# Kernel optimization log

Hardware: AMD Instinct MI355X
Metric: run time of the kernel (lower is better)

The kernel has to match this reference:

```python
import jax, jax.numpy as jnp
import numpy as np

B, CIN, COUT, H, W = 4, 256, 256, 64, 64
KH, KW = 3, 3
STRIDE, PAD = 1, 1
K = KH * KW


def setup_inputs() -> dict:
    key = jax.random.key(0)
    k1, k2, k3 = jax.random.split(key, 3)
    x = jax.random.normal(k1, (B, CIN, H, W), dtype=jnp.float32)
    # small offset weights -> offsets of O(1) pixel, realistic near init
    offset_w = jax.random.normal(k2, (2 * K, CIN, KH, KW), dtype=jnp.float32) * 0.01
    offset_b = jnp.zeros((2 * K,), dtype=jnp.float32)
    dcn_w = jax.random.normal(k3, (COUT, CIN, KH, KW), dtype=jnp.float32) * (1.0 / np.sqrt(CIN * K))
    dcn_b = jnp.zeros((COUT,), dtype=jnp.float32)
    return {"x": x, "offset_w": offset_w, "offset_b": offset_b, "dcn_w": dcn_w, "dcn_b": dcn_b}


def _conv2d(x, w, b):
    y = jax.lax.conv_general_dilated(
        x, w, window_strides=(STRIDE, STRIDE),
        padding=((PAD, PAD), (PAD, PAD)),
        dimension_numbers=("NCHW", "OIHW", "NCHW"))
    return y + b[None, :, None, None]


def _bilinear_gather(x, py, px):
    """x: [B,C,H,W]; py,px: [B,K,Ho,Wo] float sample coords.
    Zero padding outside image (torchvision deform_conv2d semantics).
    Returns [B,C,K,Ho,Wo]."""
    Bb, C, Hin, Win = x.shape
    y0 = jnp.floor(py); x0 = jnp.floor(px)
    wy1 = py - y0; wx1 = px - x0
    y0i = y0.astype(jnp.int32); x0i = x0.astype(jnp.int32)
    x_flat = x.reshape(Bb, C, Hin * Win)

    def corner(yi, xi, wgt):
        valid = (yi >= 0) & (yi < Hin) & (xi >= 0) & (xi < Win)
        yc = jnp.clip(yi, 0, Hin - 1)
        xc = jnp.clip(xi, 0, Win - 1)
        idx = (yc * Win + xc).reshape(Bb, -1)  # [B, K*Ho*Wo]
        vals = jax.vmap(lambda xf, ix: jnp.take(xf, ix, axis=1))(x_flat, idx)
        vals = vals.reshape(Bb, C, *yi.shape[1:])  # [B,C,K,Ho,Wo]
        w_eff = jnp.where(valid, wgt, 0.0)[:, None]  # [B,1,K,Ho,Wo]
        return vals * w_eff

    out = corner(y0i, x0i, (1.0 - wy1) * (1.0 - wx1))
    out = out + corner(y0i, x0i + 1, (1.0 - wy1) * wx1)
    out = out + corner(y0i + 1, x0i, wy1 * (1.0 - wx1))
    out = out + corner(y0i + 1, x0i + 1, wy1 * wx1)
    return out


def _deformable_block(x, offset_w, offset_b, dcn_w, dcn_b):
    offset = _conv2d(x, offset_w, offset_b)  # [B, 2K, Ho, Wo]
    Bb, _, Ho, Wo = offset.shape
    off = offset.reshape(Bb, K, 2, Ho, Wo)
    dy, dx = off[:, :, 0], off[:, :, 1]  # torchvision: (y, x) interleaved per tap

    ky = jnp.repeat(jnp.arange(KH), KW).astype(jnp.float32)  # [K]
    kx = jnp.tile(jnp.arange(KW), KH).astype(jnp.float32)    # [K]
    base_y = (jnp.arange(Ho, dtype=jnp.float32) * STRIDE - PAD)[None, :, None] + ky[:, None, None]  # [K,Ho,1]
    base_x = (jnp.arange(Wo, dtype=jnp.float32) * STRIDE - PAD)[None, None, :] + kx[:, None, None]  # [K,1,Wo]
    py = base_y[None] + dy  # [B,K,Ho,Wo]
    px = base_x[None] + dx

    patches = _bilinear_gather(x, py, px)  # [B,C,K,Ho,Wo]
    wk = dcn_w.reshape(COUT, CIN, K)
    out = jnp.einsum("bckhw,ock->bohw", patches, wk)
    return out + dcn_b[None, :, None, None]


def reference(x, offset_w, offset_b, dcn_w, dcn_b):
    return _deformable_block(x, offset_w, offset_b, dcn_w, dcn_b)
```

## Files before the change

kernel.cpp:

```cpp
#include <hip/hip_runtime.h>

#define BB 4
#define CIN 256
#define COUT 256
#define HH 64
#define WW 64
#define KK 9
#define OC2 18
#define KTOT (CIN * KK)

typedef __attribute__((ext_vector_type(8))) _Float16 h8;
typedef __attribute__((ext_vector_type(4))) float f32x4;

static __device__ __forceinline__ h8 splat_pk(unsigned pk) {
    union { unsigned u[4]; h8 h; } s;
    s.u[0] = pk; s.u[1] = pk; s.u[2] = pk; s.u[3] = pk;
    return s.h;
}

__global__ __launch_bounds__(256) void prework_kernel(
    const float* __restrict__ x, const float* __restrict__ ow,
    const float* __restrict__ dw,
    _Float16* __restrict__ xT, _Float16* __restrict__ bp,
    _Float16* __restrict__ bow)
{
    const int bid = blockIdx.x;
    const int t = threadIdx.x;
    if (bid < 1024) {
        const int b = bid >> 8, y = (bid >> 2) & 63, c0 = (bid & 3) * 64;
        __shared__ float tile[64][65];
#pragma unroll
        for (int r = 0; r < 16; ++r) {
            int idx = r * 256 + t;
            int c = idx >> 6, w = idx & 63;
            tile[c][w] = x[(((size_t)(b * CIN + c0 + c)) << 12) + (y << 6) + w];
        }
        __syncthreads();
        const int px = t >> 2;
#pragma unroll
        for (int half = 0; half < 2; ++half) {
            int cc = (t & 3) + half * 4;
            union { _Float16 h[8]; uint4 q; } u;
#pragma unroll
            for (int j = 0; j < 8; ++j) u.h[j] = (_Float16)tile[cc * 8 + j][px];
            size_t el = (((size_t)(b << 12)) + (y << 6) + px) * 256 + c0 + cc * 8;
            *(uint4*)&xT[el] = u.q;
        }
    } else if (bid < 1312) {
        int wid = (bid - 1024) * 256 + t;
        int T = wid >> 10;
        int r = wid & 1023;
        int cotile = r >> 6, lane = r & 63;
        int co = cotile * 16 + (lane & 15);
        int kbase = T * 32 + ((lane >> 4) & 3) * 8;
        union { _Float16 h[8]; uint4 q; } u;
#pragma unroll
        for (int j = 0; j < 8; ++j) {
            int k = kbase + j;
            int c = k & 255, kk = k >> 8;
            u.h[j] = (_Float16)dw[co * KTOT + c * KK + kk];
        }
        *(uint4*)&bp[(size_t)wid * 8] = u.q;
    } else {
        int wid = (bid - 1312) * 256 + t;
        int T = wid >> 7;
        int r = wid & 127;
        int lane = r & 63;
        int oc = ((r >> 6) << 4) + (lane & 15);
        int kbase = T * 32 + ((lane >> 4) & 3) * 8;
        union { _Float16 h[8]; uint4 q; } u;
#pragma unroll
        for (int j = 0; j < 8; ++j) {
            int k = kbase + j;
            int c = k & 255, kk = k >> 8;
            u.h[j] = (oc < OC2) ? (_Float16)ow[oc * KTOT + c * KK + kk] : (_Float16)0.f;
        }
        *(uint4*)&bow[(size_t)wid * 8] = u.q;
    }
}

__global__ __launch_bounds__(512) void offset_mfma_kernel(
    const _Float16* __restrict__ xT, const _Float16* __restrict__ bow,
    float* __restrict__ opart)
{
    const int bid = blockIdx.x;
    const int m_blk = bid >> 1, kh = bid & 1;
    const int b = m_blk >> 5;
    const int pxbase = (m_blk & 31) * 128;
    const int tid = threadIdx.x;
    const int lane = tid & 63, wv = tid >> 6;
    const int colg = lane & 15, kg = lane >> 4;

    const int pxl = pxbase + (wv << 4) + colg;
    const int py = pxl >> 6, pxx = pxl & 63;

    const _Float16* xb = xT + ((size_t)b << 20);

    auto GLOAD = [&](int T, h8& R) {
        int kk = T >> 3;
        int ky = kk / 3, kx = kk - 3 * (kk / 3);
        int yy = py + ky - 1, xx = pxx + kx - 1;
        h8 v = {0, 0, 0, 0, 0, 0, 0, 0};
        if ((unsigned)yy < HH && (unsigned)xx < WW)
            v = *(const h8*)(xb + ((((yy << 6) + xx) << 8) + ((T & 7) << 5) + (kg << 3)));
        R = v;
    };
    auto BLOAD = [&](int T, uint4* br) {
#pragma unroll
        for (int nj = 0; nj < 2; ++nj)
            br[nj] = *(const uint4*)&bow[(size_t)(((T << 1) + nj) * 64 + lane) * 8];
    };

    f32x4 acc[2];
    { f32x4 z = {0.f, 0.f, 0.f, 0.f}; acc[0] = z; acc[1] = z; }

    const int Tb = kh * 36;
    h8 E, F;
    uint4 bA[2], bB[2];

    GLOAD(Tb, E);
    BLOAD(Tb, bA);
    for (int r = 0; r < 36; r += 2) {
        GLOAD(Tb + r + 1, F);
        BLOAD(Tb + r + 1, bB);
        {
            union { uint4 q; h8 h; } u0, u1;
            u0.q = bA[0]; u1.q = bA[1];
            acc[0] = __builtin_amdgcn_mfma_f32_16x16x32_f16(E, u0.h, acc[0], 0, 0, 0);
            acc[1] = __builtin_amdgcn_mfma_f32_16x16x32_f16(E, u1.h, acc[1], 0, 0, 0);
        }
        if (r + 2 < 36) { GLOAD(Tb + r + 2, E); BLOAD(Tb + r + 2, bA); }
        {
            union { uint4 q; h8 h; } u0, u1;
            u0.q = bB[0]; u1.q = bB[1];
            acc[0] = __builtin_amdgcn_mfma_f32_16x16x32_f16(F, u0.h, acc[0], 0, 0, 0);
            acc[1] = __builtin_amdgcn_mfma_f32_16x16x32_f16(F, u1.h, acc[1], 0, 0, 0);
        }
    }

    const int pxb = pxbase + (wv << 4) + kg * 4;
#pragma unroll
    for (int nj = 0; nj < 2; ++nj) {
        int oc = nj * 16 + colg;
        if (oc < OC2) {
            float4 o;
            o.x = acc[nj][0]; o.y = acc[nj][1];
            o.z = acc[nj][2]; o.w = acc[nj][3];
            *(float4*)&opart[(((size_t)((kh * BB + b) * OC2 + oc)) << 12) + pxb] = o;
        }
    }
}

__global__ __launch_bounds__(512, 2) void dcn_mfma_kernel(
    const _Float16* __restrict__ xT, const float* __restrict__ opart,
    const float* __restrict__ ob, const _Float16* __restrict__ bp,
    const float* __restrict__ db, float* __restrict__ out)
{
    __shared__ __align__(16) _Float16 Asl[2][1088 * 8];
    __shared__ __align__(8) uint2 twp[576];
    __shared__ __align__(8) uint2 tih[576];

    int P = blockIdx.x;
    int L = (P & 7) * 64 + (P >> 3);
    const int m_blk = L >> 1, n0 = L & 1;
    const int b = m_blk >> 6;
    const int rowbase = (m_blk & 63) * 64;

    const int tid = threadIdx.x;
    const int lane = tid & 63;
    const int wn = tid >> 6;
    const int colg = lane & 15, kg = lane >> 4;

    const int g_px = tid >> 3;
    const int g_cgp = tid & 7;
    const int g_ebase = g_px * 9;
    const int g_w0 = g_px * 17 + g_cgp;

    const float* op0 = opart + (((size_t)(b * OC2)) << 12);
    const float* op1 = opart + (((size_t)((BB + b) * OC2)) << 12);
    for (int e = tid; e < 576; e += 512) {
        int p = e / 9, kk = e - (e / 9) * 9;
        int pxl = rowbase + p;
        int y = pxl >> 6, xx = pxl & 63;
        float dy = op0[((size_t)(2 * kk) << 12) + pxl]
                 + op1[((size_t)(2 * kk) << 12) + pxl] + ob[2 * kk];
        float dx = op0[((size_t)(2 * kk + 1) << 12) + pxl]
                 + op1[((size_t)(2 * kk + 1) << 12) + pxl] + ob[2 * kk + 1];
        int ky = kk / 3, kx = kk - 3 * (kk / 3);
        float sy = (float)(y - 1 + ky) + dy;
        float sx = (float)(xx - 1 + kx) + dx;
        float fy = floorf(sy), fx = floorf(sx);
        int y0 = (int)fy, x0 = (int)fx;
        float wy1 = sy - fy, wx1 = sx - fx;
        float wy0 = 1.f - wy1, wx0 = 1.f - wx1;
        bool vy0 = (unsigned)y0 < HH, vy1 = (unsigned)(y0 + 1) < HH;
        bool vx0 = (unsigned)x0 < WW, vx1 = (unsigned)(x0 + 1) < WW;
        _Float16 w00 = (_Float16)((vy0 && vx0) ? wy0 * wx0 : 0.f);
        _Float16 w01 = (_Float16)((vy0 && vx1) ? wy0 * wx1 : 0.f);
        _Float16 w10 = (_Float16)((vy1 && vx0) ? wy1 * wx0 : 0.f);
        _Float16 w11 = (_Float16)((vy1 && vx1) ? wy1 * wx1 : 0.f);
        union { _Float16 h[2]; unsigned u; } pk2;
        uint2 W;
        pk2.h[0] = w00; pk2.h[1] = w01; W.x = pk2.u;
        pk2.h[0] = w10; pk2.h[1] = w11; W.y = pk2.u;
        twp[e] = W;
        int y0c = min(max(y0, 0), HH - 1), y1c = min(max(y0 + 1, 0), HH - 1);
        int x0c = min(max(x0, 0), WW - 1), x1c = min(max(x0 + 1, 0), WW - 1);
        unsigned i00 = (unsigned)((y0c << 6) + x0c);
        unsigned i01 = (unsigned)((y0c << 6) + x1c);
        unsigned i10 = (unsigned)((y1c << 6) + x0c);
        unsigned i11 = (unsigned)((y1c << 6) + x1c);
        tih[e] = make_uint2(i00 | (i01 << 16), i10 | (i11 << 16));
    }
    __syncthreads();

    const char* xbyte = (const char*)(xT + ((size_t)b << 20));

    auto AGLOAD = [&](int st, h8* C) {
        uint2 ij = tih[g_ebase + (st >> 1)];
        unsigned chb = (unsigned)((st & 1) * 256 + g_cgp * 16);
        const char* p0 = xbyte + (((ij.x & 0xFFFFu) << 9) + chb);
        const char* p1 = xbyte + (((ij.x >> 16)     << 9) + chb);
        const char* p2 = xbyte + (((ij.y & 0xFFFFu) << 9) + chb);
        const char* p3 = xbyte + (((ij.y >> 16)     << 9) + chb);
        C[0] = *(const h8*)p0;         C[4] = *(const h8*)(p0 + 128);
        C[1] = *(const h8*)p1;         C[5] = *(const h8*)(p1 + 128);
        C[2] = *(const h8*)p2;         C[6] = *(const h8*)(p2 + 128);
        C[3] = *(const h8*)p3;         C[7] = *(const h8*)(p3 + 128);
    };
    auto GCONSUME = [&](int st, int buf, const h8* C) {
        uint2 w = twp[g_ebase + (st >> 1)];
        unsigned w00 = (w.x & 0xFFFFu) * 0x10001u;
        unsigned w01 = (w.x >> 16)     * 0x10001u;
        unsigned w10 = (w.y & 0xFFFFu) * 0x10001u;
        unsigned w11 = (w.y >> 16)     * 0x10001u;
        h8 s00 = splat_pk(w00), s01 = splat_pk(w01);
        h8 s10 = splat_pk(w10), s11 = splat_pk(w11);
        h8 v0 = C[0] * s00; v0 += C[1] * s01; v0 += C[2] * s10; v0 += C[3] * s11;
        h8 v1 = C[4] * s00; v1 += C[5] * s01; v1 += C[6] * s10; v1 += C[7] * s11;
        *(h8*)&Asl[buf][g_w0 * 8] = v0;
        *(h8*)&Asl[buf][(g_w0 + 8) * 8] = v1;
    };
    auto BLOAD = [&](int st, uint4* br) {
#pragma unroll
        for (int ks = 0; ks < 4; ++ks) {
            size_t word = ((size_t)((st * 4 + ks) * 16 + n0 * 8 + wn)) * 64 + lane;
            br[ks] = *(const uint4*)&bp[word * 8];
        }
    };

    f32x4 acc[4];
#pragma unroll
    for (int i = 0; i < 4; ++i) { f32x4 z = {0.f, 0.f, 0.f, 0.f}; acc[i] = z; }

    const int rdbase = colg * 17 + kg;
    auto MFMA16 = [&](int buf, uint4* br) {
        __builtin_amdgcn_s_setprio(1);
#pragma unroll
        for (int ks = 0; ks < 4; ++ks) {
            union { uint4 q; h8 h; } bb; bb.q = br[ks];
#pragma unroll
            for (int mi = 0; mi < 4; ++mi) {
                h8 a = *(const h8*)&Asl[buf][(mi * 272 + ks * 4 + rdbase) * 8];
                acc[mi] = __builtin_amdgcn_mfma_f32_16x16x32_f16(a, bb.h, acc[mi], 0, 0, 0);
            }
        }
        __builtin_amdgcn_s_setprio(0);
    };

    h8 C[8];
    uint4 breg[4], bnext[4];

    AGLOAD(0, C);
    BLOAD(0, breg);
    GCONSUME(0, 0, C);
    __syncthreads();

    for (int s = 0; s < 18; ++s) {
        const int cur = s & 1;
        if (s + 1 < 18) {
            BLOAD(s + 1, bnext);
            AGLOAD(s + 1, C);
        }
        MFMA16(cur, breg);
        if (s + 1 < 18) GCONSUME(s + 1, cur ^ 1, C);
        __syncthreads();
#pragma unroll
        for (int i = 0; i < 4; ++i) breg[i] = bnext[i];
    }

    const int co = n0 * 128 + wn * 16 + colg;
    const float bv = db[co];
    float* op = out + ((size_t)(b * COUT + co) << 12) + rowbase + kg * 4;
#pragma unroll
    for (int mi = 0; mi < 4; ++mi) {
        float4 o;
        o.x = acc[mi][0] + bv;
        o.y = acc[mi][1] + bv;
        o.z = acc[mi][2] + bv;
        o.w = acc[mi][3] + bv;
        *(float4*)&op[mi * 16] = o;
    }
}

extern "C" void kernel_launch(void* const* d_in, const int* in_sizes, int n_in,
                              void* d_out, int out_size, void* d_ws, size_t ws_size,
                              hipStream_t stream)
{
    const float* x  = (const float*)d_in[0];
    const float* ow = (const float*)d_in[1];
    const float* ob = (const float*)d_in[2];
    const float* dw = (const float*)d_in[3];
    const float* db = (const float*)d_in[4];
    float* out = (float*)d_out;

    char* wsp = (char*)d_ws;
    float*     opart = (float*)wsp;
    _Float16*  bp    = (_Float16*)(wsp + 2359296);
    _Float16*  bow   = (_Float16*)(wsp + 3538944);
    _Float16*  xT    = (_Float16*)(wsp + 3686400);

    hipLaunchKernelGGL(prework_kernel,     dim3(1348), dim3(256), 0, stream, x, ow, dw, xT, bp, bow);
    hipLaunchKernelGGL(offset_mfma_kernel, dim3(256),  dim3(512), 0, stream, xT, bow, opart);
    hipLaunchKernelGGL(dcn_mfma_kernel,    dim3(512),  dim3(512), 0, stream, xT, opart, ob, bp, db, out);
}
```

Baseline: 71.45 us.

## Cover full output-channel range per block to halve bilinear gather work

Each DCN block now computes all 256 output channels for its 64-pixel tile, not half of them. The grid drops from 512 to 256 blocks and each wave keeps two accumulator column tiles. Previously the bilinear gather and A-tile build for each pixel tile ran twice, once per channel half; now it runs once and feeds twice as many MFMAs. The shared A layout also changes from a padded stride to an XOR swizzle to avoid bank conflicts, at the cost of more registers per thread and fewer blocks for latency hiding.

```diff
diff --git a/kernel.cpp b/kernel.cpp
--- a/kernel.cpp
+++ b/kernel.cpp
@@ -156,15 +156,14 @@
     const float* __restrict__ ob, const _Float16* __restrict__ bp,
     const float* __restrict__ db, float* __restrict__ out)
 {
-    __shared__ __align__(16) _Float16 Asl[2][1088 * 8];
+    __shared__ __align__(16) _Float16 Asl[2][1024 * 8];
     __shared__ __align__(8) uint2 twp[576];
     __shared__ __align__(8) uint2 tih[576];
 
     int P = blockIdx.x;
-    int L = (P & 7) * 64 + (P >> 3);
-    const int m_blk = L >> 1, n0 = L & 1;
-    const int b = m_blk >> 6;
-    const int rowbase = (m_blk & 63) * 64;
+    int L = (P & 7) * 32 + (P >> 3);
+    const int b = L >> 6;
+    const int rowbase = (L & 63) * 64;
 
     const int tid = threadIdx.x;
     const int lane = tid & 63;
@@ -174,7 +173,8 @@
     const int g_px = tid >> 3;
     const int g_cgp = tid & 7;
     const int g_ebase = g_px * 9;
-    const int g_w0 = g_px * 17 + g_cgp;
+    const int g_w0 = g_cgp * 64 + (g_px ^ g_cgp);
+    const int g_w1 = (g_cgp + 8) * 64 + (g_px ^ g_cgp);
 
     const float* op0 = opart + (((size_t)(b * OC2)) << 12);
     const float* op1 = opart + (((size_t)((BB + b) * OC2)) << 12);
@@ -239,37 +239,44 @@
         h8 v0 = C[0] * s00; v0 += C[1] * s01; v0 += C[2] * s10; v0 += C[3] * s11;
         h8 v1 = C[4] * s00; v1 += C[5] * s01; v1 += C[6] * s10; v1 += C[7] * s11;
         *(h8*)&Asl[buf][g_w0 * 8] = v0;
-        *(h8*)&Asl[buf][(g_w0 + 8) * 8] = v1;
+        *(h8*)&Asl[buf][g_w1 * 8] = v1;
     };
     auto BLOAD = [&](int st, uint4* br) {
 #pragma unroll
+        for (int ks = 0; ks < 4; ++ks)
+#pragma unroll
+            for (int nj = 0; nj < 2; ++nj) {
+                size_t word = ((size_t)((st * 4 + ks) * 16 + wn * 2 + nj)) * 64 + lane;
+                br[ks * 2 + nj] = *(const uint4*)&bp[word * 8];
+            }
+    };
+
+    f32x4 acc[4][2];
+#pragma unroll
+    for (int mi = 0; mi < 4; ++mi)
+#pragma unroll
+        for (int nj = 0; nj < 2; ++nj) { f32x4 z = {0.f,0.f,0.f,0.f}; acc[mi][nj] = z; }
+
+    auto MFMA32 = [&](int buf, uint4* br) {
+        __builtin_amdgcn_s_setprio(1);
+#pragma unroll
         for (int ks = 0; ks < 4; ++ks) {
-            size_t word = ((size_t)((st * 4 + ks) * 16 + n0 * 8 + wn)) * 64 + lane;
-            br[ks] = *(const uint4*)&bp[word * 8];
-        }
-    };
-
-    f32x4 acc[4];
-#pragma unroll
-    for (int i = 0; i < 4; ++i) { f32x4 z = {0.f, 0.f, 0.f, 0.f}; acc[i] = z; }
-
-    const int rdbase = colg * 17 + kg;
-    auto MFMA16 = [&](int buf, uint4* br) {
-        __builtin_amdgcn_s_setprio(1);
-#pragma unroll
-        for (int ks = 0; ks < 4; ++ks) {
-            union { uint4 q; h8 h; } bb; bb.q = br[ks];
+            const int cg = ks * 4 + kg;
+            union { uint4 q; h8 h; } b0, b1;
+            b0.q = br[ks * 2]; b1.q = br[ks * 2 + 1];
 #pragma unroll
             for (int mi = 0; mi < 4; ++mi) {
-                h8 a = *(const h8*)&Asl[buf][(mi * 272 + ks * 4 + rdbase) * 8];
-                acc[mi] = __builtin_amdgcn_mfma_f32_16x16x32_f16(a, bb.h, acc[mi], 0, 0, 0);
+                int w = cg * 64 + ((mi * 16 + colg) ^ (cg & 7));
+                h8 a = *(const h8*)&Asl[buf][w * 8];
+                acc[mi][0] = __builtin_amdgcn_mfma_f32_16x16x32_f16(a, b0.h, acc[mi][0], 0, 0, 0);
+                acc[mi][1] = __builtin_amdgcn_mfma_f32_16x16x32_f16(a, b1.h, acc[mi][1], 0, 0, 0);
             }
         }
         __builtin_amdgcn_s_setprio(0);
     };
 
     h8 C[8];
-    uint4 breg[4], bnext[4];
+    uint4 breg[8], bnext[8];
 
     AGLOAD(0, C);
     BLOAD(0, breg);
@@ -279,27 +286,30 @@
     for (int s = 0; s < 18; ++s) {
         const int cur = s & 1;
         if (s + 1 < 18) {
+            AGLOAD(s + 1, C);
             BLOAD(s + 1, bnext);
-            AGLOAD(s + 1, C);
-        }
-        MFMA16(cur, breg);
+        }
+        MFMA32(cur, breg);
         if (s + 1 < 18) GCONSUME(s + 1, cur ^ 1, C);
         __syncthreads();
 #pragma unroll
-        for (int i = 0; i < 4; ++i) breg[i] = bnext[i];
-    }
-
-    const int co = n0 * 128 + wn * 16 + colg;
-    const float bv = db[co];
-    float* op = out + ((size_t)(b * COUT + co) << 12) + rowbase + kg * 4;
-#pragma unroll
-    for (int mi = 0; mi < 4; ++mi) {
-        float4 o;
-        o.x = acc[mi][0] + bv;
-        o.y = acc[mi][1] + bv;
-        o.z = acc[mi][2] + bv;
-        o.w = acc[mi][3] + bv;
-        *(float4*)&op[mi * 16] = o;
+        for (int i = 0; i < 8; ++i) breg[i] = bnext[i];
+    }
+
+#pragma unroll
+    for (int nj = 0; nj < 2; ++nj) {
+        const int co = wn * 32 + nj * 16 + colg;
+        const float bv = db[co];
+        float* op = out + ((size_t)(b * COUT + co) << 12) + rowbase + kg * 4;
+#pragma unroll
+        for (int mi = 0; mi < 4; ++mi) {
+            float4 o;
+            o.x = acc[mi][nj][0] + bv;
+            o.y = acc[mi][nj][1] + bv;
+            o.z = acc[mi][nj][2] + bv;
+            o.w = acc[mi][nj][3] + bv;
+            *(float4*)&op[mi * 16] = o;
+        }
     }
 }
 
@@ -322,5 +332,5 @@
 
     hipLaunchKernelGGL(prework_kernel,     dim3(1348), dim3(256), 0, stream, x, ow, dw, xT, bp, bow);
     hipLaunchKernelGGL(offset_mfma_kernel, dim3(256),  dim3(512), 0, stream, xT, bow, opart);
-    hipLaunchKernelGGL(dcn_mfma_kernel,    dim3(512),  dim3(512), 0, stream, xT, opart, ob, bp, db, out);
-}
+    hipLaunchKernelGGL(dcn_mfma_kernel,    dim3(256),  dim3(512), 0, stream, xT, opart, ob, bp, db, out);
+}
```

Result: no change. 71.24 us (-0.3%).
